# Kernel tuning notes

Measured on AMD Instinct MI355X. Metric: run time of the kernel, lower is better.

## Reference

```python
import jax, jax.numpy as jnp
from jax import lax
import numpy as np

NUM_KIND = 4
V, H, B = 34, 32, 4096   # raw vertical (2 rows dropped), horizontal, batch
KS = 33                  # odd-rounded max(V-2, H)
NUM_DEPTH = 4
N_SQ = 100


def _conv(x, w):
    # x: (N,1,h,w), w: (1,1,KS,KS); torch Conv2d == cross-correlation == lax default
    return lax.conv_general_dilated(x, w, (1, 1), 'SAME',
                                    dimension_numbers=('NCHW', 'OIHW', 'NCHW'))


def _conv_k(x, w):
    # x: (K,B,1,h,w) -> conv each map with the shared 1-channel kernel
    k, b, c, h, wd = x.shape
    return _conv(x.reshape(k * b, c, h, wd), w).reshape(k, b, c, h, wd)


def setup_inputs() -> dict:
    key = jax.random.key(0)
    ks = jax.random.split(key, 8)
    std = 0.3
    return {
        'dots':    jax.random.randint(ks[0], (V, H, B), 0, NUM_KIND + 1, dtype=jnp.int32),
        'w_each':  jax.random.normal(ks[1], (1, 1, KS, KS), jnp.float32) * std,
        'w_not':   jax.random.normal(ks[2], (1, 1, KS, KS), jnp.float32) * std,
        'w_not2':  jax.random.normal(ks[3], (1, 1, KS, KS), jnp.float32) * std,
        'w_empty': jax.random.normal(ks[4], (1, 1, KS, KS), jnp.float32) * std,
        'W1':      jax.random.normal(ks[5], (N_SQ, (V - 2) * H), jnp.float32) * std,
        'W2':      jax.random.normal(ks[6], (N_SQ, N_SQ), jnp.float32) * std,
        'W3':      jax.random.normal(ks[7], (1, N_SQ), jnp.float32) * std,
    }


def reference(dots, w_each, w_not, w_not2, w_empty, W1, W2, W3):
    # drop last 2 vertical rows, layout (V-2,H,B) -> (B,1,V-2,H)
    board = dots[:-2].astype(jnp.float32).transpose(2, 0, 1)[:, None]  # (B,1,h,w)

    empty = (board == 0).astype(jnp.float32)
    E = _conv(empty, w_empty)                                           # (B,1,h,w)

    kinds = jnp.arange(1, NUM_KIND + 1, dtype=board.dtype).reshape(NUM_KIND, 1, 1, 1, 1)
    each = (board[None] == kinds).astype(jnp.float32)                   # (K,B,1,h,w)
    notm = ((each + empty[None]) == 0).astype(jnp.float32)              # (K,B,1,h,w)

    # first pass: per-color value, masked to that color's cells
    notm_conv = _conv_k(notm, w_not)      # note: the torch code LOGS the convolved not-mask
    v = _conv_k(each, w_each) + E[None] - notm_conv
    L = each * v                          # each_color_value_log (masked)
    s = jax.nn.sigmoid(L.sum(axis=0))     # all_color_value_2nd, (B,1,h,w)

    # iterative diffusion; torch mutates the log in-place each depth:
    # L <- mask * (L + E + conv2nd(notm_conv * before)); before is detached
    for _ in range(NUM_DEPTH):
        before = lax.stop_gradient(s)
        C = _conv_k(notm_conv * before[None], w_not2)
        L = each * (L + E[None] + C)
        s = jax.nn.sigmoid(L.sum(axis=0))

    feat = s.reshape(s.shape[0], -1)      # (B, (V-2)*H)
    x = jax.nn.leaky_relu(feat @ W1.T, 0.2)
    x = jax.nn.leaky_relu(x @ W2.T, 0.2)
    return x @ W3.T                        # (B,1)
```

## Files before the change

kernel.cpp:

```cpp
#include <hip/hip_runtime.h>
#include <cstdint>
#include <cstddef>


typedef _Float16 f16;
typedef __attribute__((ext_vector_type(8))) _Float16 f16x8;
typedef __attribute__((ext_vector_type(4))) float f32x4;

#define NB   4096
#define PIX  1024
#define MR   (NB * 4)

__device__ __forceinline__ void gld_lds16(const void* g, void* l) {
    __builtin_amdgcn_global_load_lds(
        (const __attribute__((address_space(1))) void*)g,
        (__attribute__((address_space(3))) void*)l, 16, 0, 0);
}

__global__ void build_mats(const float* __restrict__ we, const float* __restrict__ wn,
                           const float* __restrict__ wn2, const float* __restrict__ wem,
                           f16* __restrict__ Me, f16* __restrict__ Mn,
                           f16* __restrict__ Mn2, f16* __restrict__ Mem) {
    int idx = blockIdx.x * 256 + threadIdx.x;
    int o = idx >> 10, in = idx & 1023;
    int i = o >> 5, j = o & 31, a = in >> 5, b = in & 31;
    int u = a - i + 16, v = b - j + 16;
    bool ok = (u >= 0) && (u < 33) && (v >= 0) && (v < 33);
    int w = u * 33 + v;
    float ve = 0.f, vn = 0.f, vn2 = 0.f, vem = 0.f;
    if (ok) { ve = we[w]; vn = wn[w]; vn2 = wn2[w]; vem = wem[w]; }
    Me[idx]  = (f16)ve;
    Mn[idx]  = (f16)vn;
    Mn2[idx] = (f16)vn2;
    Mem[idx] = (f16)vem;
}

__global__ void build_w1(const float* __restrict__ W1, f16* __restrict__ W1b) {
    int idx = blockIdx.x * 256 + threadIdx.x;
    int j = idx >> 10, i = idx & 1023;
    W1b[idx] = (f16)(j < 100 ? W1[j * 1024 + i] : 0.f);
}

__global__ void build_board(const int* __restrict__ dots, unsigned char* __restrict__ board) {
    __shared__ unsigned char tile[64][68];
    int t = threadIdx.x;
    int bp = blockIdx.x & 15, bn = blockIdx.x >> 4;
    int p0 = bp * 64, n0 = bn * 64;
    int ln = t & 63, lp = t >> 6;
#pragma unroll
    for (int j = 0; j < 16; j++) {
        int p = lp * 16 + j;
        tile[p][ln] = (unsigned char)dots[(size_t)(p0 + p) * 4096 + n0 + ln];
    }
    __syncthreads();
#pragma unroll
    for (int j = 0; j < 16; j++) {
        int n = lp * 16 + j;
        board[(size_t)(n0 + n) * 1024 + p0 + ln] = tile[ln][n];
    }
}

template <int MODE, int ASRC>
__global__ void __launch_bounds__(256, 2) gemm_k(
    const f16* __restrict__ X, const f16* __restrict__ Mt, int K, int ypx,
    const f16* __restrict__ NCs, const f16* __restrict__ Sin,
    const unsigned char* __restrict__ board, const f16* __restrict__ En,
    float* __restrict__ Lsel, f16* __restrict__ outB, int ldo,
    float* __restrict__ outF) {
    __shared__ __attribute__((aligned(16))) char smem[32768];
    char* smA = smem;
    char* smB = smem + 16384;
    const int tid = threadIdx.x;
    const int wv = tid >> 6, ln = tid & 63;
    const int wm = wv >> 1, wn_ = wv & 1;
    const int lr = ln & 15, lq = ln >> 4;

    int bi = blockIdx.x, bx, by;
    if (ypx > 0) {
        int xcd = bi & 7, slot = bi >> 3;
        bx = slot & 7;
        by = xcd * ypx + (slot >> 3);
    } else {
        bx = 0; by = bi;
    }
    const int rtile = by * 128, otile = bx * 128;

    const f32x4 fz = {0.f, 0.f, 0.f, 0.f};
    f32x4 acc[4][4];
#pragma unroll
    for (int i = 0; i < 4; i++)
#pragma unroll
        for (int j = 0; j < 4; j++) acc[i][j] = fz;

    for (int kb = 0; kb < K; kb += 64) {
#pragma unroll
        for (int t = 0; t < 4; t++) {
            int c = (wv * 4 + t) * 64 + ln;
            int row = c >> 3;
            int gcol = (c & 7) ^ (row & 7);
            int gr = rtile + row;
            int gk = kb + gcol * 8;
            if (ASRC == 0) {
                gld_lds16(X + (size_t)gr * K + gk, smA + (wv * 4 + t) * 1024);
            } else if (ASRC == 1) {
                f16x8 nc = *(const f16x8*)(NCs + (size_t)gr * PIX + gk);
                f16x8 sv = *(const f16x8*)(Sin + (size_t)(gr >> 2) * PIX + gk);
                *(f16x8*)(smA + c * 16) = nc * sv;
            } else {
                int n = (ASRC == 4) ? gr : (gr >> 2);
                uint64_t bb = *(const uint64_t*)(board + (size_t)n * PIX + gk);
                int k1 = (gr & 3) + 1;
                f16x8 v;
#pragma unroll
                for (int j = 0; j < 8; j++) {
                    int bj = (int)((bb >> (8 * j)) & 0xff);
                    bool on = (ASRC == 2) ? (bj == k1)
                            : (ASRC == 3) ? (bj != 0 && bj != k1)
                                          : (bj == 0);
                    v[j] = on ? (f16)1.f : (f16)0.f;
                }
                *(f16x8*)(smA + c * 16) = v;
            }
            gld_lds16(Mt + (size_t)(otile + row) * K + gk, smB + (wv * 4 + t) * 1024);
        }
        __syncthreads();
#pragma unroll
        for (int kk = 0; kk < 2; kk++) {
            f16x8 af[4], bfr[4];
#pragma unroll
            for (int i = 0; i < 4; i++) {
                int rrow = wm * 64 + i * 16 + lr;
                int phys = (kk * 4 + lq) ^ (rrow & 7);
                af[i] = *(const f16x8*)(smA + rrow * 128 + phys * 16);
            }
#pragma unroll
            for (int j = 0; j < 4; j++) {
                int brow = wn_ * 64 + j * 16 + lr;
                int phys = (kk * 4 + lq) ^ (brow & 7);
                bfr[j] = *(const f16x8*)(smB + brow * 128 + phys * 16);
            }
#pragma unroll
            for (int i = 0; i < 4; i++)
#pragma unroll
                for (int j = 0; j < 4; j++)
                    acc[i][j] = __builtin_amdgcn_mfma_f32_16x16x32_f16(
                        af[i], bfr[j], acc[i][j], 0, 0, 0);
        }
        __syncthreads();
    }

#pragma unroll
    for (int i = 0; i < 4; i++) {
        int rbase = rtile + wm * 64 + i * 16 + lq * 4;
#pragma unroll
        for (int j = 0; j < 4; j++) {
            int o = otile + wn_ * 64 + j * 16 + lr;
            f32x4 a = acc[i][j];
            if (MODE == 0) {
#pragma unroll
                for (int v = 0; v < 4; v++)
                    outB[(size_t)(rbase + v) * ldo + o] = (f16)a[v];
            } else if (MODE == 5) {
#pragma unroll
                for (int v = 0; v < 4; v++) {
                    float x = a[v];
                    outF[(size_t)(rbase + v) * ldo + o] = x > 0.f ? x : 0.2f * x;
                }
            } else {
                int n = rbase >> 2;
                size_t no = (size_t)n * PIX + o;
                int c = board[no];
                float E = (float)En[no];
                float asel = (c == 1) ? a[0] : (c == 2) ? a[1] : (c == 3) ? a[2] : a[3];
                float Lnew;
                if (MODE == 2) {
                    float ncsel = (float)NCs[(size_t)(rbase + (c > 0 ? c - 1 : 0)) * PIX + o];
                    Lnew = (c > 0) ? (asel + E - ncsel) : 0.f;
                } else {
                    Lnew = (c > 0) ? (Lsel[no] + E + asel) : 0.f;
                }
                float s = 1.f / (1.f + expf(-Lnew));
                if (MODE != 4) Lsel[no] = Lnew;
                outB[no] = (f16)s;
            }
        }
    }
}

__global__ void __launch_bounds__(256) mlp23(const float* __restrict__ X1,
                                             const float* __restrict__ W2,
                                             const float* __restrict__ W3,
                                             float* __restrict__ out) {
    __shared__ float sW2[10000];
    __shared__ float sW3[100];
    __shared__ float red[256];
    int t = threadIdx.x;
    for (int idx = t; idx < 10000; idx += 256) sW2[idx] = W2[idx];
    if (t < 100) sW3[t] = W3[t];
    __syncthreads();
    int nb = t >> 2, q = t & 3;
    int n = blockIdx.x * 64 + nb;
    const float* x1 = X1 + (size_t)n * 128;
    float xr[100];
#pragma unroll
    for (int i = 0; i < 100; i++) xr[i] = x1[i];
    float partial = 0.f;
    for (int jj = 0; jj < 25; jj++) {
        int j = q + jj * 4;
        const float* w2r = sW2 + j * 100;
        float acc2 = 0.f;
#pragma unroll
        for (int i = 0; i < 100; i++) acc2 += w2r[i] * xr[i];
        partial += sW3[j] * (acc2 > 0.f ? acc2 : 0.2f * acc2);
    }
    red[t] = partial;
    __syncthreads();
    if (q == 0) out[n] = red[t] + red[t + 1] + red[t + 2] + red[t + 3];
}

extern "C" void kernel_launch(void* const* d_in, const int* in_sizes, int n_in,
                              void* d_out, int out_size, void* d_ws, size_t ws_size,
                              hipStream_t stream) {
    (void)in_sizes; (void)n_in; (void)out_size; (void)ws_size;
    const int*   dots   = (const int*)d_in[0];
    const float* w_each = (const float*)d_in[1];
    const float* w_not  = (const float*)d_in[2];
    const float* w_not2 = (const float*)d_in[3];
    const float* w_emp  = (const float*)d_in[4];
    const float* W1 = (const float*)d_in[5];
    const float* W2 = (const float*)d_in[6];
    const float* W3 = (const float*)d_in[7];
    float* out = (float*)d_out;

    char* ws = (char*)d_ws;
    size_t off = 0;
    auto alloc = [&](size_t bytes) -> char* {
        char* p = ws + off;
        off += (bytes + 255) & ~(size_t)255;
        return p;
    };
    f16* Me   = (f16*)alloc((size_t)PIX * PIX * 2);
    f16* Mn   = (f16*)alloc((size_t)PIX * PIX * 2);
    f16* Mn2  = (f16*)alloc((size_t)PIX * PIX * 2);
    f16* Mem  = (f16*)alloc((size_t)PIX * PIX * 2);
    f16* W1b  = (f16*)alloc((size_t)128 * PIX * 2);
    unsigned char* board = (unsigned char*)alloc((size_t)NB * PIX);
    f16*   NC   = (f16*)alloc((size_t)MR * PIX * 2);
    f16*   En   = (f16*)alloc((size_t)NB * PIX * 2);
    f16*   Sa   = (f16*)alloc((size_t)NB * PIX * 2);
    f16*   Sb   = (f16*)alloc((size_t)NB * PIX * 2);
    f16*   feat = (f16*)alloc((size_t)NB * PIX * 2);
    float* Lsel = (float*)alloc((size_t)NB * PIX * 4);
    float* X1   = (float*)alloc((size_t)NB * 128 * 4);

    build_mats<<<4096, 256, 0, stream>>>(w_each, w_not, w_not2, w_emp, Me, Mn, Mn2, Mem);
    build_w1<<<512, 256, 0, stream>>>(W1, W1b);
    build_board<<<1024, 256, 0, stream>>>(dots, board);

    dim3 blk(256);
    gemm_k<0, 3><<<1024, blk, 0, stream>>>(nullptr, Mn, 1024, 16, nullptr, nullptr,
                                           board, nullptr, nullptr, NC, PIX, nullptr);
    gemm_k<0, 4><<<256, blk, 0, stream>>>(nullptr, Mem, 1024, 4, nullptr, nullptr,
                                          board, nullptr, nullptr, En, PIX, nullptr);
    gemm_k<2, 2><<<1024, blk, 0, stream>>>(nullptr, Me, 1024, 16, NC, nullptr,
                                           board, En, Lsel, Sa, 0, nullptr);
    gemm_k<3, 1><<<1024, blk, 0, stream>>>(nullptr, Mn2, 1024, 16, NC, Sa,
                                           board, En, Lsel, Sb, 0, nullptr);
    gemm_k<3, 1><<<1024, blk, 0, stream>>>(nullptr, Mn2, 1024, 16, NC, Sb,
                                           board, En, Lsel, Sa, 0, nullptr);
    gemm_k<3, 1><<<1024, blk, 0, stream>>>(nullptr, Mn2, 1024, 16, NC, Sa,
                                           board, En, Lsel, Sb, 0, nullptr);
    gemm_k<4, 1><<<1024, blk, 0, stream>>>(nullptr, Mn2, 1024, 16, NC, Sb,
                                           board, En, Lsel, feat, 0, nullptr);
    gemm_k<5, 0><<<32, blk, 0, stream>>>(feat, W1b, 1024, 0, nullptr, nullptr,
                                         nullptr, nullptr, nullptr, nullptr, 128, X1);
    mlp23<<<64, blk, 0, stream>>>(X1, W2, W3, out);
}
```

Baseline: 432.1 us.

## Widen GEMM tiles to 128x256, use 32x32 MFMA, expand masks from LDS

The GEMM kernel is templated on N-tile width, so the main convolution-as-GEMM launches use 128x256 tiles with 32x32x16 MFMA instructions instead of 128x128 tiles with 16x16x32. The A operand is built from LDS: the board bytes and the S vector are loaded once per tile via direct global-to-LDS copies, and the masks or the NC*S product are formed when fragments are read. Fewer, larger blocks are meant to cut redundant A-side loads and per-element mask building in global memory. The cost is more accumulator registers and LDS per block, which may lower occupancy under the 2-blocks launch bound. expf is also replaced by __expf.

```diff
diff --git a/kernel.cpp b/kernel.cpp
--- a/kernel.cpp
+++ b/kernel.cpp
@@ -5,7 +5,7 @@
 
 typedef _Float16 f16;
 typedef __attribute__((ext_vector_type(8))) _Float16 f16x8;
-typedef __attribute__((ext_vector_type(4))) float f32x4;
+typedef __attribute__((ext_vector_type(16))) float f32x16;
 
 #define NB   4096
 #define PIX  1024
@@ -60,128 +60,170 @@
     }
 }
 
-template <int MODE, int ASRC>
+template <int MODE, int ASRC, int NT>
 __global__ void __launch_bounds__(256, 2) gemm_k(
-    const f16* __restrict__ X, const f16* __restrict__ Mt, int K, int ypx,
+    const f16* __restrict__ X, const f16* __restrict__ Mt, int ypx, int nx,
     const f16* __restrict__ NCs, const f16* __restrict__ Sin,
     const unsigned char* __restrict__ board, const f16* __restrict__ En,
     float* __restrict__ Lsel, f16* __restrict__ outB, int ldo,
     float* __restrict__ outF) {
-    __shared__ __attribute__((aligned(16))) char smem[32768];
-    char* smA = smem;
-    char* smB = smem + 16384;
+    constexpr int BN = NT * 64;
+    constexpr int SMB = BN * 128;
+    constexpr int SMA = (ASRC == 0) ? 128 * 128
+                      : (ASRC == 1) ? (128 * 128 + 32 * 128)
+                      : (ASRC == 4) ? 128 * 64
+                                    : 32 * 64;
+    __shared__ __attribute__((aligned(16))) char smem[SMB + SMA];
+    char* smB = smem;
+    char* smA = smem + SMB;
+    char* smS = smA + 128 * 128;
+
     const int tid = threadIdx.x;
     const int wv = tid >> 6, ln = tid & 63;
     const int wm = wv >> 1, wn_ = wv & 1;
-    const int lr = ln & 15, lq = ln >> 4;
-
-    int bi = blockIdx.x, bx, by;
-    if (ypx > 0) {
-        int xcd = bi & 7, slot = bi >> 3;
-        bx = slot & 7;
-        by = xcd * ypx + (slot >> 3);
-    } else {
-        bx = 0; by = bi;
-    }
-    const int rtile = by * 128, otile = bx * 128;
-
-    const f32x4 fz = {0.f, 0.f, 0.f, 0.f};
-    f32x4 acc[4][4];
-#pragma unroll
-    for (int i = 0; i < 4; i++)
-#pragma unroll
-        for (int j = 0; j < 4; j++) acc[i][j] = fz;
-
-    for (int kb = 0; kb < K; kb += 64) {
-#pragma unroll
-        for (int t = 0; t < 4; t++) {
-            int c = (wv * 4 + t) * 64 + ln;
-            int row = c >> 3;
-            int gcol = (c & 7) ^ (row & 7);
-            int gr = rtile + row;
-            int gk = kb + gcol * 8;
-            if (ASRC == 0) {
-                gld_lds16(X + (size_t)gr * K + gk, smA + (wv * 4 + t) * 1024);
-            } else if (ASRC == 1) {
-                f16x8 nc = *(const f16x8*)(NCs + (size_t)gr * PIX + gk);
-                f16x8 sv = *(const f16x8*)(Sin + (size_t)(gr >> 2) * PIX + gk);
-                *(f16x8*)(smA + c * 16) = nc * sv;
-            } else {
-                int n = (ASRC == 4) ? gr : (gr >> 2);
-                uint64_t bb = *(const uint64_t*)(board + (size_t)n * PIX + gk);
-                int k1 = (gr & 3) + 1;
-                f16x8 v;
-#pragma unroll
-                for (int j = 0; j < 8; j++) {
-                    int bj = (int)((bb >> (8 * j)) & 0xff);
-                    bool on = (ASRC == 2) ? (bj == k1)
-                            : (ASRC == 3) ? (bj != 0 && bj != k1)
-                                          : (bj == 0);
-                    v[j] = on ? (f16)1.f : (f16)0.f;
-                }
-                *(f16x8*)(smA + c * 16) = v;
-            }
-            gld_lds16(Mt + (size_t)(otile + row) * K + gk, smB + (wv * 4 + t) * 1024);
+    const int lc = ln & 31, h = ln >> 5;
+
+    int bi = blockIdx.x;
+    int xcd = bi & 7, slot = bi >> 3;
+    int bx = slot % nx;
+    int by = xcd * ypx + slot / nx;
+    const int rtile = by * 128, otile = bx * BN;
+    const int img0 = (ASRC == 4) ? rtile : (rtile >> 2);
+
+    f32x16 acc[2][NT];
+#pragma unroll
+    for (int i = 0; i < 2; i++)
+#pragma unroll
+        for (int j = 0; j < NT; j++)
+#pragma unroll
+            for (int v = 0; v < 16; v++) acc[i][j][v] = 0.f;
+
+    for (int kb = 0; kb < 1024; kb += 64) {
+#pragma unroll
+        for (int s0 = wv * 64; s0 < BN * 8; s0 += 256) {
+            int slot_ = s0 + ln, row = slot_ >> 3;
+            int gcol = (slot_ & 7) ^ (row & 7);
+            gld_lds16(Mt + (size_t)(otile + row) * 1024 + kb + gcol * 8,
+                      smB + s0 * 16);
+        }
+        if (ASRC == 0) {
+#pragma unroll
+            for (int s0 = wv * 64; s0 < 1024; s0 += 256) {
+                int slot_ = s0 + ln, row = slot_ >> 3;
+                int gcol = (slot_ & 7) ^ (row & 7);
+                gld_lds16(X + (size_t)(rtile + row) * 1024 + kb + gcol * 8,
+                          smA + s0 * 16);
+            }
+        } else if (ASRC == 1) {
+#pragma unroll
+            for (int s0 = wv * 64; s0 < 1024; s0 += 256) {
+                int slot_ = s0 + ln, row = slot_ >> 3;
+                int gcol = (slot_ & 7) ^ (row & 7);
+                gld_lds16(NCs + (size_t)(rtile + row) * 1024 + kb + gcol * 8,
+                          smA + s0 * 16);
+            }
+            {
+                int slot_ = wv * 64 + ln, row = slot_ >> 3;
+                int gcol = (slot_ & 7) ^ (row & 7);
+                gld_lds16(Sin + (size_t)(img0 + row) * 1024 + kb + gcol * 8,
+                          smS + wv * 64 * 16);
+            }
+        } else {
+            constexpr int BSLOTS = (ASRC == 4) ? 512 : 128;
+#pragma unroll
+            for (int s0 = wv * 64; s0 < BSLOTS; s0 += 256) {
+                int slot_ = s0 + ln, row = slot_ >> 2;
+                int gc = (slot_ & 3) ^ (row & 3);
+                gld_lds16(board + (size_t)(img0 + row) * 1024 + kb + gc * 16,
+                          smA + s0 * 16);
+            }
         }
         __syncthreads();
-#pragma unroll
-        for (int kk = 0; kk < 2; kk++) {
-            f16x8 af[4], bfr[4];
-#pragma unroll
-            for (int i = 0; i < 4; i++) {
-                int rrow = wm * 64 + i * 16 + lr;
-                int phys = (kk * 4 + lq) ^ (rrow & 7);
-                af[i] = *(const f16x8*)(smA + rrow * 128 + phys * 16);
-            }
-#pragma unroll
-            for (int j = 0; j < 4; j++) {
-                int brow = wn_ * 64 + j * 16 + lr;
-                int phys = (kk * 4 + lq) ^ (brow & 7);
-                bfr[j] = *(const f16x8*)(smB + brow * 128 + phys * 16);
-            }
-#pragma unroll
-            for (int i = 0; i < 4; i++)
-#pragma unroll
-                for (int j = 0; j < 4; j++)
-                    acc[i][j] = __builtin_amdgcn_mfma_f32_16x16x32_f16(
-                        af[i], bfr[j], acc[i][j], 0, 0, 0);
+
+#pragma unroll
+        for (int kk = 0; kk < 4; kk++) {
+            const int oct = kk * 2 + h;
+            f16x8 af[2], bf[NT];
+#pragma unroll
+            for (int i = 0; i < 2; i++) {
+                int m = wm * 64 + i * 32 + lc;
+                if (ASRC == 0) {
+                    af[i] = *(const f16x8*)(smA + m * 128 + ((oct) ^ (m & 7)) * 16);
+                } else if (ASRC == 1) {
+                    f16x8 nc = *(const f16x8*)(smA + m * 128 + ((oct) ^ (m & 7)) * 16);
+                    int img = m >> 2;
+                    f16x8 sv = *(const f16x8*)(smS + img * 128 + ((oct) ^ (img & 7)) * 16);
+                    af[i] = nc * sv;
+                } else {
+                    int row = (ASRC == 4) ? m : (m >> 2);
+                    int k1 = (m & 3) + 1;
+                    uint64_t bb = *(const uint64_t*)(smA + row * 64 +
+                                   (((oct >> 1)) ^ (row & 3)) * 16 + (oct & 1) * 8);
+                    f16x8 v;
+#pragma unroll
+                    for (int jj = 0; jj < 8; jj++) {
+                        int bj = (int)((bb >> (8 * jj)) & 0xff);
+                        bool on = (ASRC == 2) ? (bj == k1)
+                                : (ASRC == 3) ? (bj != 0 && bj != k1)
+                                              : (bj == 0);
+                        v[jj] = on ? (f16)1.f : (f16)0.f;
+                    }
+                    af[i] = v;
+                }
+            }
+#pragma unroll
+            for (int j = 0; j < NT; j++) {
+                int bn = wn_ * (NT * 32) + j * 32 + lc;
+                bf[j] = *(const f16x8*)(smB + bn * 128 + ((oct) ^ (bn & 7)) * 16);
+            }
+#pragma unroll
+            for (int i = 0; i < 2; i++)
+#pragma unroll
+                for (int j = 0; j < NT; j++)
+                    acc[i][j] = __builtin_amdgcn_mfma_f32_32x32x16_f16(
+                        af[i], bf[j], acc[i][j], 0, 0, 0);
         }
         __syncthreads();
     }
 
 #pragma unroll
-    for (int i = 0; i < 4; i++) {
-        int rbase = rtile + wm * 64 + i * 16 + lq * 4;
-#pragma unroll
-        for (int j = 0; j < 4; j++) {
-            int o = otile + wn_ * 64 + j * 16 + lr;
-            f32x4 a = acc[i][j];
-            if (MODE == 0) {
-#pragma unroll
-                for (int v = 0; v < 4; v++)
-                    outB[(size_t)(rbase + v) * ldo + o] = (f16)a[v];
-            } else if (MODE == 5) {
-#pragma unroll
-                for (int v = 0; v < 4; v++) {
-                    float x = a[v];
-                    outF[(size_t)(rbase + v) * ldo + o] = x > 0.f ? x : 0.2f * x;
+    for (int i = 0; i < 2; i++) {
+        int rb = rtile + wm * 64 + i * 32;
+#pragma unroll
+        for (int j = 0; j < NT; j++) {
+            int o = otile + wn_ * (NT * 32) + j * 32 + lc;
+            f32x16 a = acc[i][j];
+#pragma unroll
+            for (int q = 0; q < 4; q++) {
+                int rr = rb + 8 * q + 4 * h;
+                if (MODE == 0) {
+#pragma unroll
+                    for (int v = 0; v < 4; v++)
+                        outB[(size_t)(rr + v) * ldo + o] = (f16)a[4 * q + v];
+                } else if (MODE == 5) {
+#pragma unroll
+                    for (int v = 0; v < 4; v++) {
+                        float x = a[4 * q + v];
+                        outF[(size_t)(rr + v) * ldo + o] = x > 0.f ? x : 0.2f * x;
+                    }
+                } else {
+                    int n = rr >> 2;
+                    size_t no = (size_t)n * PIX + o;
+                    int c = board[no];
+                    float E = (float)En[no];
+                    float asel = (c == 1) ? a[4 * q] : (c == 2) ? a[4 * q + 1]
+                               : (c == 3) ? a[4 * q + 2] : a[4 * q + 3];
+                    float Lnew;
+                    if (MODE == 2) {
+                        float ncsel = (float)NCs[(size_t)(4 * n + (c > 0 ? c - 1 : 0)) * PIX + o];
+                        Lnew = (c > 0) ? (asel + E - ncsel) : 0.f;
+                    } else {
+                        Lnew = (c > 0) ? (Lsel[no] + E + asel) : 0.f;
+                    }
+                    float s = 1.f / (1.f + __expf(-Lnew));
+                    if (MODE != 4) Lsel[no] = Lnew;
+                    outB[no] = (f16)s;
                 }
-            } else {
-                int n = rbase >> 2;
-                size_t no = (size_t)n * PIX + o;
-                int c = board[no];
-                float E = (float)En[no];
-                float asel = (c == 1) ? a[0] : (c == 2) ? a[1] : (c == 3) ? a[2] : a[3];
-                float Lnew;
-                if (MODE == 2) {
-                    float ncsel = (float)NCs[(size_t)(rbase + (c > 0 ? c - 1 : 0)) * PIX + o];
-                    Lnew = (c > 0) ? (asel + E - ncsel) : 0.f;
-                } else {
-                    Lnew = (c > 0) ? (Lsel[no] + E + asel) : 0.f;
-                }
-                float s = 1.f / (1.f + expf(-Lnew));
-                if (MODE != 4) Lsel[no] = Lnew;
-                outB[no] = (f16)s;
             }
         }
     }
@@ -258,21 +300,21 @@
     build_board<<<1024, 256, 0, stream>>>(dots, board);
 
     dim3 blk(256);
-    gemm_k<0, 3><<<1024, blk, 0, stream>>>(nullptr, Mn, 1024, 16, nullptr, nullptr,
-                                           board, nullptr, nullptr, NC, PIX, nullptr);
-    gemm_k<0, 4><<<256, blk, 0, stream>>>(nullptr, Mem, 1024, 4, nullptr, nullptr,
-                                          board, nullptr, nullptr, En, PIX, nullptr);
-    gemm_k<2, 2><<<1024, blk, 0, stream>>>(nullptr, Me, 1024, 16, NC, nullptr,
-                                           board, En, Lsel, Sa, 0, nullptr);
-    gemm_k<3, 1><<<1024, blk, 0, stream>>>(nullptr, Mn2, 1024, 16, NC, Sa,
-                                           board, En, Lsel, Sb, 0, nullptr);
-    gemm_k<3, 1><<<1024, blk, 0, stream>>>(nullptr, Mn2, 1024, 16, NC, Sb,
-                                           board, En, Lsel, Sa, 0, nullptr);
-    gemm_k<3, 1><<<1024, blk, 0, stream>>>(nullptr, Mn2, 1024, 16, NC, Sa,
-                                           board, En, Lsel, Sb, 0, nullptr);
-    gemm_k<4, 1><<<1024, blk, 0, stream>>>(nullptr, Mn2, 1024, 16, NC, Sb,
-                                           board, En, Lsel, feat, 0, nullptr);
-    gemm_k<5, 0><<<32, blk, 0, stream>>>(feat, W1b, 1024, 0, nullptr, nullptr,
-                                         nullptr, nullptr, nullptr, nullptr, 128, X1);
+    gemm_k<0, 3, 4><<<512, blk, 0, stream>>>(nullptr, Mn, 16, 4, nullptr, nullptr,
+                                             board, nullptr, nullptr, NC, PIX, nullptr);
+    gemm_k<0, 4, 4><<<128, blk, 0, stream>>>(nullptr, Mem, 4, 4, nullptr, nullptr,
+                                             board, nullptr, nullptr, En, PIX, nullptr);
+    gemm_k<2, 2, 4><<<512, blk, 0, stream>>>(nullptr, Me, 16, 4, NC, nullptr,
+                                             board, En, Lsel, Sa, 0, nullptr);
+    gemm_k<3, 1, 4><<<512, blk, 0, stream>>>(nullptr, Mn2, 16, 4, NC, Sa,
+                                             board, En, Lsel, Sb, 0, nullptr);
+    gemm_k<3, 1, 4><<<512, blk, 0, stream>>>(nullptr, Mn2, 16, 4, NC, Sb,
+                                             board, En, Lsel, Sa, 0, nullptr);
+    gemm_k<3, 1, 4><<<512, blk, 0, stream>>>(nullptr, Mn2, 16, 4, NC, Sa,
+                                             board, En, Lsel, Sb, 0, nullptr);
+    gemm_k<4, 1, 4><<<512, blk, 0, stream>>>(nullptr, Mn2, 16, 4, NC, Sb,
+                                             board, En, Lsel, feat, 0, nullptr);
+    gemm_k<5, 0, 2><<<32, blk, 0, stream>>>(feat, W1b, 4, 1, nullptr, nullptr,
+                                            nullptr, nullptr, nullptr, nullptr, 128, X1);
     mlp23<<<64, blk, 0, stream>>>(X1, W2, W3, out);
 }
```

New measurement: 453.1 us. 1.05x slower.

## Fold first-pass not-mask conv algebraically and fuse initial GEMMs into one launch

Applied to the files above, without the earlier changes.

Rewrites the first-pass value as conv(each, we+wn) + conv(empty, wem+wn) - conv(ones, wn), using a stacked K=2048 weight matrix and a precomputed row-sum vector tn. This drops the first pass's dependency on the NC buffer, so the first-pass, NC and En GEMMs can run as one combined launch. All A-operand sources (board bytes, NC and S tiles) are now staged into LDS with async global-to-LDS loads, and the mask and product are formed at fragment-read time. The change also raises launch bounds to 4 blocks per CU and switches to __expf. The trade-off is twice the K-depth for the first-pass GEMM and extra LDS use, which may limit occupancy.

```diff
diff --git a/kernel.cpp b/kernel.cpp
--- a/kernel.cpp
+++ b/kernel.cpp
@@ -19,8 +19,8 @@
 
 __global__ void build_mats(const float* __restrict__ we, const float* __restrict__ wn,
                            const float* __restrict__ wn2, const float* __restrict__ wem,
-                           f16* __restrict__ Me, f16* __restrict__ Mn,
-                           f16* __restrict__ Mn2, f16* __restrict__ Mem) {
+                           f16* __restrict__ Mn, f16* __restrict__ Mn2,
+                           f16* __restrict__ Mem, f16* __restrict__ Bst) {
     int idx = blockIdx.x * 256 + threadIdx.x;
     int o = idx >> 10, in = idx & 1023;
     int i = o >> 5, j = o & 31, a = in >> 5, b = in & 31;
@@ -29,10 +29,22 @@
     int w = u * 33 + v;
     float ve = 0.f, vn = 0.f, vn2 = 0.f, vem = 0.f;
     if (ok) { ve = we[w]; vn = wn[w]; vn2 = wn2[w]; vem = wem[w]; }
-    Me[idx]  = (f16)ve;
     Mn[idx]  = (f16)vn;
     Mn2[idx] = (f16)vn2;
     Mem[idx] = (f16)vem;
+    Bst[(size_t)o * 2048 + in]        = (f16)(ve + vn);
+    Bst[(size_t)o * 2048 + 1024 + in] = (f16)(vem + vn);
+}
+
+__global__ void tn_build(const f16* __restrict__ Mn, float* __restrict__ tn) {
+    int o = blockIdx.x * 256 + threadIdx.x;
+    float s = 0.f;
+    for (int j = 0; j < 128; j++) {
+        f16x8 v = *(const f16x8*)(Mn + (size_t)o * 1024 + j * 8);
+#pragma unroll
+        for (int e = 0; e < 8; e++) s += (float)v[e];
+    }
+    tn[o] = s;
 }
 
 __global__ void build_w1(const float* __restrict__ W1, f16* __restrict__ W1b) {
@@ -61,29 +73,27 @@
 }
 
 template <int MODE, int ASRC>
-__global__ void __launch_bounds__(256, 2) gemm_k(
-    const f16* __restrict__ X, const f16* __restrict__ Mt, int K, int ypx,
-    const f16* __restrict__ NCs, const f16* __restrict__ Sin,
-    const unsigned char* __restrict__ board, const f16* __restrict__ En,
-    float* __restrict__ Lsel, f16* __restrict__ outB, int ldo,
-    float* __restrict__ outF) {
-    __shared__ __attribute__((aligned(16))) char smem[32768];
-    char* smA = smem;
-    char* smB = smem + 16384;
+__device__ __forceinline__ void run_gemm(
+    int bjob, int ypx, int nx, char* smem,
+    const f16* __restrict__ X, const f16* __restrict__ B, int K,
+    const unsigned char* __restrict__ board, const f16* __restrict__ NCs,
+    const f16* __restrict__ Sin, const f16* __restrict__ En,
+    const float* __restrict__ tn, float* __restrict__ Lsel,
+    f16* __restrict__ outB, int ldo, float* __restrict__ outF) {
+    char* smB = smem;
+    char* smA = smem + 16384;
+    char* smS = smem + 32768;
+
     const int tid = threadIdx.x;
     const int wv = tid >> 6, ln = tid & 63;
     const int wm = wv >> 1, wn_ = wv & 1;
     const int lr = ln & 15, lq = ln >> 4;
 
-    int bi = blockIdx.x, bx, by;
-    if (ypx > 0) {
-        int xcd = bi & 7, slot = bi >> 3;
-        bx = slot & 7;
-        by = xcd * ypx + (slot >> 3);
-    } else {
-        bx = 0; by = bi;
-    }
+    int xcd = bjob & 7, slot = bjob >> 3;
+    int bx = slot % nx;
+    int by = xcd * ypx + slot / nx;
     const int rtile = by * 128, otile = bx * 128;
+    const int img0 = (ASRC == 4) ? rtile : (rtile >> 2);
 
     const f32x4 fz = {0.f, 0.f, 0.f, 0.f};
     f32x4 acc[4][4];
@@ -95,49 +105,84 @@
     for (int kb = 0; kb < K; kb += 64) {
 #pragma unroll
         for (int t = 0; t < 4; t++) {
-            int c = (wv * 4 + t) * 64 + ln;
-            int row = c >> 3;
-            int gcol = (c & 7) ^ (row & 7);
-            int gr = rtile + row;
-            int gk = kb + gcol * 8;
-            if (ASRC == 0) {
-                gld_lds16(X + (size_t)gr * K + gk, smA + (wv * 4 + t) * 1024);
-            } else if (ASRC == 1) {
-                f16x8 nc = *(const f16x8*)(NCs + (size_t)gr * PIX + gk);
-                f16x8 sv = *(const f16x8*)(Sin + (size_t)(gr >> 2) * PIX + gk);
-                *(f16x8*)(smA + c * 16) = nc * sv;
-            } else {
-                int n = (ASRC == 4) ? gr : (gr >> 2);
-                uint64_t bb = *(const uint64_t*)(board + (size_t)n * PIX + gk);
-                int k1 = (gr & 3) + 1;
-                f16x8 v;
-#pragma unroll
-                for (int j = 0; j < 8; j++) {
-                    int bj = (int)((bb >> (8 * j)) & 0xff);
-                    bool on = (ASRC == 2) ? (bj == k1)
-                            : (ASRC == 3) ? (bj != 0 && bj != k1)
-                                          : (bj == 0);
-                    v[j] = on ? (f16)1.f : (f16)0.f;
-                }
-                *(f16x8*)(smA + c * 16) = v;
-            }
-            gld_lds16(Mt + (size_t)(otile + row) * K + gk, smB + (wv * 4 + t) * 1024);
+            int c = t * 256 + wv * 64 + ln;
+            int row = c >> 3, gcol = (c & 7) ^ (row & 7);
+            gld_lds16(B + (size_t)(otile + row) * K + kb + gcol * 8, smB + c * 16);
+        }
+        if (ASRC == 0) {
+#pragma unroll
+            for (int t = 0; t < 4; t++) {
+                int c = t * 256 + wv * 64 + ln;
+                int row = c >> 3, gcol = (c & 7) ^ (row & 7);
+                gld_lds16(X + (size_t)(rtile + row) * K + kb + gcol * 8, smA + c * 16);
+            }
+        } else if (ASRC == 1) {
+#pragma unroll
+            for (int t = 0; t < 4; t++) {
+                int c = t * 256 + wv * 64 + ln;
+                int row = c >> 3, gcol = (c & 7) ^ (row & 7);
+                gld_lds16(NCs + (size_t)(rtile + row) * 1024 + kb + gcol * 8, smA + c * 16);
+            }
+            {
+                int c = wv * 64 + ln;
+                int row = c >> 3, gcol = (c & 7) ^ (row & 7);
+                gld_lds16(Sin + (size_t)(img0 + row) * 1024 + kb + gcol * 8, smS + c * 16);
+            }
+        } else if (ASRC == 4) {
+            int cb = kb;
+#pragma unroll
+            for (int t = 0; t < 2; t++) {
+                int c = t * 256 + wv * 64 + ln;
+                int row = c >> 2, g = (c & 3) ^ (row & 3);
+                gld_lds16(board + (size_t)(img0 + row) * 1024 + cb + g * 16, smA + c * 16);
+            }
+        } else {
+            int cb = (ASRC == 5) ? (kb & 1023) : kb;
+            if (wv < 2) {
+                int c = wv * 64 + ln;
+                int row = c >> 2, g = (c & 3) ^ (row & 3);
+                gld_lds16(board + (size_t)(img0 + row) * 1024 + cb + g * 16, smA + c * 16);
+            }
         }
         __syncthreads();
+
 #pragma unroll
         for (int kk = 0; kk < 2; kk++) {
+            const int oct = kk * 4 + lq;
             f16x8 af[4], bfr[4];
 #pragma unroll
             for (int i = 0; i < 4; i++) {
                 int rrow = wm * 64 + i * 16 + lr;
-                int phys = (kk * 4 + lq) ^ (rrow & 7);
-                af[i] = *(const f16x8*)(smA + rrow * 128 + phys * 16);
+                if (ASRC == 0) {
+                    af[i] = *(const f16x8*)(smA + rrow * 128 + (oct ^ (rrow & 7)) * 16);
+                } else if (ASRC == 1) {
+                    f16x8 nc = *(const f16x8*)(smA + rrow * 128 + (oct ^ (rrow & 7)) * 16);
+                    int img = rrow >> 2;
+                    f16x8 sv = *(const f16x8*)(smS + img * 128 + (oct ^ (img & 7)) * 16);
+                    af[i] = nc * sv;
+                } else {
+                    int m = (ASRC == 4) ? rrow : (rrow >> 2);
+                    int k1 = (rrow & 3) + 1;
+                    uint64_t bb = *(const uint64_t*)(smA + m * 64 +
+                                    (((oct >> 1)) ^ (m & 3)) * 16 + (oct & 1) * 8);
+                    bool ext = (ASRC == 5) && (kb >= 1024);
+                    f16x8 v;
+#pragma unroll
+                    for (int jj = 0; jj < 8; jj++) {
+                        int bj = (int)((bb >> (8 * jj)) & 0xff);
+                        bool on = (ASRC == 4) ? (bj == 0)
+                                : (ASRC == 3) ? (bj != 0 && bj != k1)
+                                : ext          ? (bj == 0)
+                                               : (bj == k1);
+                        v[jj] = on ? (f16)1.f : (f16)0.f;
+                    }
+                    af[i] = v;
+                }
             }
 #pragma unroll
             for (int j = 0; j < 4; j++) {
                 int brow = wn_ * 64 + j * 16 + lr;
-                int phys = (kk * 4 + lq) ^ (brow & 7);
-                bfr[j] = *(const f16x8*)(smB + brow * 128 + phys * 16);
+                bfr[j] = *(const f16x8*)(smB + brow * 128 + (oct ^ (brow & 7)) * 16);
             }
 #pragma unroll
             for (int i = 0; i < 4; i++)
@@ -170,21 +215,58 @@
                 int n = rbase >> 2;
                 size_t no = (size_t)n * PIX + o;
                 int c = board[no];
-                float E = (float)En[no];
                 float asel = (c == 1) ? a[0] : (c == 2) ? a[1] : (c == 3) ? a[2] : a[3];
                 float Lnew;
                 if (MODE == 2) {
-                    float ncsel = (float)NCs[(size_t)(rbase + (c > 0 ? c - 1 : 0)) * PIX + o];
-                    Lnew = (c > 0) ? (asel + E - ncsel) : 0.f;
+                    Lnew = (c > 0) ? (asel - tn[o]) : 0.f;
                 } else {
+                    float E = (float)En[no];
                     Lnew = (c > 0) ? (Lsel[no] + E + asel) : 0.f;
                 }
-                float s = 1.f / (1.f + expf(-Lnew));
+                float s = 1.f / (1.f + __expf(-Lnew));
                 if (MODE != 4) Lsel[no] = Lnew;
                 outB[no] = (f16)s;
             }
         }
     }
+}
+
+__global__ void __launch_bounds__(256, 4) gemm_fa(
+    const f16* __restrict__ Bst, const f16* __restrict__ Mn,
+    const f16* __restrict__ Mem, const unsigned char* __restrict__ board,
+    const float* __restrict__ tn, float* __restrict__ Lsel,
+    f16* __restrict__ Sa, f16* __restrict__ NC, f16* __restrict__ En) {
+    __shared__ __attribute__((aligned(16))) char smem[24576];
+    int bi = blockIdx.x;
+    if (bi < 1024) {
+        run_gemm<2, 5>(bi, 16, 8, smem, nullptr, Bst, 2048, board, nullptr,
+                       nullptr, nullptr, tn, Lsel, Sa, 0, nullptr);
+    } else if (bi < 2048) {
+        run_gemm<0, 3>(bi - 1024, 16, 8, smem, nullptr, Mn, 1024, board, nullptr,
+                       nullptr, nullptr, nullptr, nullptr, NC, PIX, nullptr);
+    } else {
+        run_gemm<0, 4>(bi - 2048, 4, 8, smem, nullptr, Mem, 1024, board, nullptr,
+                       nullptr, nullptr, nullptr, nullptr, En, PIX, nullptr);
+    }
+}
+
+template <int MODE>
+__global__ void __launch_bounds__(256, 4) gemm_depth(
+    const f16* __restrict__ Mn2, const unsigned char* __restrict__ board,
+    const f16* __restrict__ NCs, const f16* __restrict__ Sin,
+    const f16* __restrict__ En, float* __restrict__ Lsel,
+    f16* __restrict__ outB) {
+    __shared__ __attribute__((aligned(16))) char smem[36864];
+    run_gemm<MODE, 1>(blockIdx.x, 16, 8, smem, nullptr, Mn2, 1024, board, NCs,
+                      Sin, En, nullptr, Lsel, outB, 0, nullptr);
+}
+
+__global__ void __launch_bounds__(256, 4) gemm_mlp(
+    const f16* __restrict__ feat, const f16* __restrict__ W1b,
+    float* __restrict__ X1) {
+    __shared__ __attribute__((aligned(16))) char smem[32768];
+    run_gemm<5, 0>(blockIdx.x, 4, 1, smem, feat, W1b, 1024, nullptr, nullptr,
+                   nullptr, nullptr, nullptr, nullptr, nullptr, 128, X1);
 }
 
 __global__ void __launch_bounds__(256) mlp23(const float* __restrict__ X1,
@@ -239,10 +321,10 @@
         off += (bytes + 255) & ~(size_t)255;
         return p;
     };
-    f16* Me   = (f16*)alloc((size_t)PIX * PIX * 2);
     f16* Mn   = (f16*)alloc((size_t)PIX * PIX * 2);
     f16* Mn2  = (f16*)alloc((size_t)PIX * PIX * 2);
     f16* Mem  = (f16*)alloc((size_t)PIX * PIX * 2);
+    f16* Bst  = (f16*)alloc((size_t)PIX * 2048 * 2);
     f16* W1b  = (f16*)alloc((size_t)128 * PIX * 2);
     unsigned char* board = (unsigned char*)alloc((size_t)NB * PIX);
     f16*   NC   = (f16*)alloc((size_t)MR * PIX * 2);
@@ -251,28 +333,20 @@
     f16*   Sb   = (f16*)alloc((size_t)NB * PIX * 2);
     f16*   feat = (f16*)alloc((size_t)NB * PIX * 2);
     float* Lsel = (float*)alloc((size_t)NB * PIX * 4);
+    float* tn   = (float*)alloc((size_t)PIX * 4);
     float* X1   = (float*)alloc((size_t)NB * 128 * 4);
 
-    build_mats<<<4096, 256, 0, stream>>>(w_each, w_not, w_not2, w_emp, Me, Mn, Mn2, Mem);
+    build_mats<<<4096, 256, 0, stream>>>(w_each, w_not, w_not2, w_emp, Mn, Mn2, Mem, Bst);
+    tn_build<<<4, 256, 0, stream>>>(Mn, tn);
     build_w1<<<512, 256, 0, stream>>>(W1, W1b);
     build_board<<<1024, 256, 0, stream>>>(dots, board);
 
     dim3 blk(256);
-    gemm_k<0, 3><<<1024, blk, 0, stream>>>(nullptr, Mn, 1024, 16, nullptr, nullptr,
-                                           board, nullptr, nullptr, NC, PIX, nullptr);
-    gemm_k<0, 4><<<256, blk, 0, stream>>>(nullptr, Mem, 1024, 4, nullptr, nullptr,
-                                          board, nullptr, nullptr, En, PIX, nullptr);
-    gemm_k<2, 2><<<1024, blk, 0, stream>>>(nullptr, Me, 1024, 16, NC, nullptr,
-                                           board, En, Lsel, Sa, 0, nullptr);
-    gemm_k<3, 1><<<1024, blk, 0, stream>>>(nullptr, Mn2, 1024, 16, NC, Sa,
-                                           board, En, Lsel, Sb, 0, nullptr);
-    gemm_k<3, 1><<<1024, blk, 0, stream>>>(nullptr, Mn2, 1024, 16, NC, Sb,
-                                           board, En, Lsel, Sa, 0, nullptr);
-    gemm_k<3, 1><<<1024, blk, 0, stream>>>(nullptr, Mn2, 1024, 16, NC, Sa,
-                                           board, En, Lsel, Sb, 0, nullptr);
-    gemm_k<4, 1><<<1024, blk, 0, stream>>>(nullptr, Mn2, 1024, 16, NC, Sb,
-                                           board, En, Lsel, feat, 0, nullptr);
-    gemm_k<5, 0><<<32, blk, 0, stream>>>(feat, W1b, 1024, 0, nullptr, nullptr,
-                                         nullptr, nullptr, nullptr, nullptr, 128, X1);
+    gemm_fa<<<2304, blk, 0, stream>>>(Bst, Mn, Mem, board, tn, Lsel, Sa, NC, En);
+    gemm_depth<3><<<1024, blk, 0, stream>>>(Mn2, board, NC, Sa, En, Lsel, Sb);
+    gemm_depth<3><<<1024, blk, 0, stream>>>(Mn2, board, NC, Sb, En, Lsel, Sa);
+    gemm_depth<3><<<1024, blk, 0, stream>>>(Mn2, board, NC, Sa, En, Lsel, Sb);
+    gemm_depth<4><<<1024, blk, 0, stream>>>(Mn2, board, NC, Sb, En, Lsel, feat);
+    gemm_mlp<<<32, blk, 0, stream>>>(feat, W1b, X1);
     mlp23<<<64, blk, 0, stream>>>(X1, W2, W3, out);
 }
```

After: 433.1 us. About the same (+0.2%).
